# Kernel tuning notes

Measured on AMD Instinct MI355X. Metric: run time of the kernel, lower is better.

Reference implementation:

```python
import jax, jax.numpy as jnp
import numpy as np
import math

B, S, E = 2, 2048, 1024
NH, NKV, HD = 16, 4, 64
GATE_CH = 12

def _rope(x, cos, sin):
    h = x.shape[-1] // 2
    x1, x2 = x[..., :h], x[..., h:]
    return jnp.concatenate((x1 * cos + x2 * sin, x1 * -sin + x2 * cos), axis=-1)

def _rms_norm(x):
    eps = jnp.finfo(x.dtype).eps
    return x * jax.lax.rsqrt(jnp.mean(x * x, axis=-1, keepdims=True) + eps)

def setup_inputs() -> dict:
    key = jax.random.key(0)
    ks = jax.random.split(key, 9)
    x = jax.random.normal(ks[0], (B, S, E), dtype=jnp.float32)
    ve = jax.random.normal(ks[1], (B, S, NKV * HD), dtype=jnp.float32)
    t = jnp.arange(S, dtype=jnp.float32)[:, None]
    inv_freq = 1.0 / (10000.0 ** (jnp.arange(0, HD // 2, dtype=jnp.float32) / (HD // 2)))
    ang = t * inv_freq[None, :]
    cos = jnp.cos(ang)[None, :, None, :]  # (1,S,1,HD//2)
    sin = jnp.sin(ang)[None, :, None, :]
    attn_mask = jnp.tril(jnp.ones((S, S), dtype=bool))[None, None]  # causal (1,1,S,S)
    sc = 0.02
    Wq = jax.random.normal(ks[2], (NH * HD, E), dtype=jnp.float32) * sc
    Wk = jax.random.normal(ks[3], (NKV * HD, E), dtype=jnp.float32) * sc
    Wv = jax.random.normal(ks[4], (NKV * HD, E), dtype=jnp.float32) * sc
    Wproj = jax.random.normal(ks[5], (E, E), dtype=jnp.float32) * sc
    Wgate = jax.random.normal(ks[6], (NKV, GATE_CH), dtype=jnp.float32) * sc
    return {"x": x, "ve": ve, "cos": cos, "sin": sin, "attn_mask": attn_mask,
            "Wq": Wq, "Wk": Wk, "Wv": Wv, "Wproj": Wproj, "Wgate": Wgate}

def reference(x, ve, cos, sin, attn_mask, Wq, Wk, Wv, Wproj, Wgate):
    b, s, _ = x.shape
    q = (x @ Wq.T).reshape(b, s, NH, HD)
    k = (x @ Wk.T).reshape(b, s, NKV, HD)
    v = (x @ Wv.T).reshape(b, s, NKV, HD)
    # value-embedding gating
    gate = 3.0 * jax.nn.sigmoid(x[..., :GATE_CH] @ Wgate.T)  # (b,s,NKV)
    v = v + gate[..., None] * ve.reshape(b, s, NKV, HD)
    # RoPE + QK-RMSNorm
    q = _rms_norm(_rope(q, cos, sin)) * 1.2
    k = _rms_norm(_rope(k, cos, sin)) * 1.2
    # GQA: repeat KV heads
    rep = NH // NKV
    k = jnp.repeat(k, rep, axis=2)
    v = jnp.repeat(v, rep, axis=2)
    q = q.transpose(0, 2, 1, 3)  # (b,h,s,d)
    k = k.transpose(0, 2, 1, 3)
    v = v.transpose(0, 2, 1, 3)
    scores = jnp.einsum('bhqd,bhkd->bhqk', q, k) / math.sqrt(HD)
    scores = jnp.where(attn_mask, scores, jnp.finfo(scores.dtype).min)
    attn = jax.nn.softmax(scores, axis=-1)
    y = jnp.einsum('bhqk,bhkd->bhqd', attn, v)
    y = y.transpose(0, 2, 1, 3).reshape(b, s, NH * HD)
    return y @ Wproj.T
```

## Files before the change

kernel.cpp:

```cpp
#include <hip/hip_runtime.h>
#include <hip/hip_bf16.h>
#include <math.h>

typedef short bf16x8 __attribute__((ext_vector_type(8)));
typedef float f32x4 __attribute__((ext_vector_type(4)));

#define LROW 72
#define NSPLIT 3

__device__ __forceinline__ unsigned short f2bf(float f) {
  union { float f; unsigned int u; } v; v.f = f;
  unsigned int u = v.u;
  unsigned int r = (u + 0x7fffu + ((u >> 16) & 1u)) >> 16;
  return (unsigned short)r;
}
__device__ __forceinline__ float bf2f(unsigned short u) {
  return __uint_as_float((unsigned)u << 16);
}

#if __has_builtin(__builtin_amdgcn_global_load_lds)
#define HAVE_GLD 1
__device__ __forceinline__ void gld16(const void* g, void* l) {
  __builtin_amdgcn_global_load_lds(
      (const __attribute__((address_space(1))) unsigned int*)g,
      (__attribute__((address_space(3))) unsigned int*)l, 16, 0, 0);
}
#else
#define HAVE_GLD 0
#endif

__global__ __launch_bounds__(256) void cvt_all_kernel(const float* __restrict__ x,
                                                      const float* __restrict__ Wq,
                                                      const float* __restrict__ Wk,
                                                      const float* __restrict__ Wv,
                                                      const float* __restrict__ Wproj,
                                                      unsigned short* __restrict__ xb,
                                                      unsigned short* __restrict__ wqkv,
                                                      unsigned short* __restrict__ wpj) {
  int blk = blockIdx.x;
  const float* src;
  unsigned short* dst;
  if (blk < 4096)      { src = x + (size_t)blk * 1024;            dst = xb + (size_t)blk * 1024; }
  else if (blk < 5120) { src = Wq + (size_t)(blk - 4096) * 1024;  dst = wqkv + (size_t)(blk - 4096) * 1024; }
  else if (blk < 5376) { src = Wk + (size_t)(blk - 5120) * 1024;  dst = wqkv + (size_t)(blk - 4096) * 1024; }
  else if (blk < 5632) { src = Wv + (size_t)(blk - 5376) * 1024;  dst = wqkv + (size_t)(blk - 4096) * 1024; }
  else                 { src = Wproj + (size_t)(blk - 5632) * 1024; dst = wpj + (size_t)(blk - 5632) * 1024; }
  int i = threadIdx.x;
  float4 v = ((const float4*)src)[i];
  ushort4 o;
  o.x = f2bf(v.x); o.y = f2bf(v.y); o.z = f2bf(v.z); o.w = f2bf(v.w);
  ((ushort4*)dst)[i] = o;
}

__global__ __launch_bounds__(256) void gemm_qkv_kernel(const unsigned short* __restrict__ A,
                                                       const unsigned short* __restrict__ B,
                                                       const float* __restrict__ ve,
                                                       const float* __restrict__ cosb,
                                                       const float* __restrict__ sinb,
                                                       const float* __restrict__ wgate,
                                                       unsigned short* __restrict__ Q,
                                                       unsigned short* __restrict__ Kd,
                                                       unsigned short* __restrict__ Vt) {
  __shared__ unsigned short As[64 * 64];
  __shared__ unsigned short Bs[128 * 64];
  __shared__ float gLDS[128];
  const int K = 1024;
  int tid = threadIdx.x;
  int wave = tid >> 6, lane = tid & 63, l15 = lane & 15, quad = lane >> 4;
  int wm = (wave >> 1) * 32, wn = (wave & 1) * 64;
  int n0 = blockIdx.x * 128, m0 = blockIdx.y * 64;
  if (n0 >= 1280 && tid < 128) {
    int rl = tid & 63, khl = tid >> 6;
    int kh = ((n0 >> 6) - 20) + khl;
    float dot = 0.f;
#pragma unroll
    for (int jj = 0; jj < 12; jj++)
      dot += bf2f(A[(size_t)(m0 + rl) * 1024 + jj]) * wgate[kh * 12 + jj];
    gLDS[khl * 64 + rl] = 3.0f / (1.0f + __expf(-dot));
  }
  f32x4 acc[2][4];
#pragma unroll
  for (int i = 0; i < 2; i++)
#pragma unroll
    for (int j = 0; j < 4; j++) acc[i][j] = (f32x4){0.f, 0.f, 0.f, 0.f};
  int srow = lane >> 3;
  int scol = ((lane & 7) ^ srow) * 8;
  for (int k0 = 0; k0 < K; k0 += 64) {
    __syncthreads();
#if HAVE_GLD
#pragma unroll
    for (int j = 0; j < 2; j++) {
      int row = wave * 16 + j * 8;
      gld16(A + (size_t)(m0 + row + srow) * K + k0 + scol, As + row * 64 + lane * 8);
    }
#pragma unroll
    for (int j = 0; j < 4; j++) {
      int row = wave * 32 + j * 8;
      gld16(B + (size_t)(n0 + row + srow) * K + k0 + scol, Bs + row * 64 + lane * 8);
    }
#else
#pragma unroll
    for (int j = 0; j < 2; j++) {
      int row = wave * 16 + j * 8;
      *(float4*)(As + row * 64 + lane * 8) = *(const float4*)(A + (size_t)(m0 + row + srow) * K + k0 + scol);
    }
#pragma unroll
    for (int j = 0; j < 4; j++) {
      int row = wave * 32 + j * 8;
      *(float4*)(Bs + row * 64 + lane * 8) = *(const float4*)(B + (size_t)(n0 + row + srow) * K + k0 + scol);
    }
#endif
    __syncthreads();
#pragma unroll
    for (int s = 0; s < 2; s++) {
      bf16x8 af[2], bf[4];
#pragma unroll
      for (int i = 0; i < 2; i++)
        af[i] = *(const bf16x8*)(As + (wm + i * 16 + l15) * 64 + (((s * 4 + quad) ^ (l15 & 7)) * 8));
#pragma unroll
      for (int j = 0; j < 4; j++)
        bf[j] = *(const bf16x8*)(Bs + (wn + j * 16 + l15) * 64 + (((s * 4 + quad) ^ (l15 & 7)) * 8));
#pragma unroll
      for (int i = 0; i < 2; i++)
#pragma unroll
        for (int j = 0; j < 4; j++)
          acc[i][j] = __builtin_amdgcn_mfma_f32_16x16x32_bf16(af[i], bf[j], acc[i][j], 0, 0, 0);
    }
  }
  int hs = (n0 + wn) >> 6;
  if (hs < 20) {
    bool isq = hs < 16;
    float postscale = isq ? 0.216404256f : 1.2f;
#pragma unroll
    for (int i = 0; i < 2; i++) {
#pragma unroll
      for (int r = 0; r < 4; r++) {
        int row = m0 + wm + i * 16 + quad * 4 + r;
        int s = row & 2047, b = row >> 11;
        float c0 = cosb[s * 32 + l15],      s0 = sinb[s * 32 + l15];
        float c1 = cosb[s * 32 + 16 + l15], s1 = sinb[s * 32 + 16 + l15];
        float v0 = acc[i][0][r], v1 = acc[i][1][r], v2 = acc[i][2][r], v3 = acc[i][3][r];
        float n0v = fmaf(v0, c0,  v2 * s0);
        float n1v = fmaf(v1, c1,  v3 * s1);
        float n2v = fmaf(v2, c0, -v0 * s0);
        float n3v = fmaf(v3, c1, -v1 * s1);
        float ss = (n0v * n0v + n1v * n1v) + (n2v * n2v + n3v * n3v);
        ss += __shfl_xor(ss, 1, 64); ss += __shfl_xor(ss, 2, 64);
        ss += __shfl_xor(ss, 4, 64); ss += __shfl_xor(ss, 8, 64);
        float sc = rsqrtf(ss * (1.0f / 64.0f) + 1.1920929e-07f) * postscale;
        unsigned short* dp = isq ? Q + ((size_t)(b * 16 + hs) * 2048 + s) * 64
                                 : Kd + ((size_t)(b * 4 + hs - 16) * 2048 + s) * 64;
        dp[l15]      = f2bf(n0v * sc);
        dp[16 + l15] = f2bf(n1v * sc);
        dp[32 + l15] = f2bf(n2v * sc);
        dp[48 + l15] = f2bf(n3v * sc);
      }
    }
  } else {
    int kh = hs - 20;
#pragma unroll
    for (int i = 0; i < 2; i++) {
#pragma unroll
      for (int r = 0; r < 4; r++) {
        int rl = wm + i * 16 + quad * 4 + r;
        int row = m0 + rl, s = row & 2047, b = row >> 11;
        float g = gLDS[(wave & 1) * 64 + rl];
        const float* vep = ve + (size_t)row * 256 + kh * 64;
        unsigned short* vp = Vt + ((size_t)(b * 4 + kh) * 64) * 2048 + s;
#pragma unroll
        for (int j = 0; j < 4; j++) {
          float vv = fmaf(g, vep[j * 16 + l15], acc[i][j][r]);
          vp[(size_t)(j * 16 + l15) * 2048] = f2bf(vv);
        }
      }
    }
  }
}

__global__ __launch_bounds__(256) void flash_kernel(const unsigned short* __restrict__ Q,
                                                    const unsigned short* __restrict__ K,
                                                    const unsigned short* __restrict__ Vt,
                                                    unsigned short* __restrict__ accP,
                                                    float* __restrict__ lP) {
  __shared__ unsigned short Ks[64 * 64];
  __shared__ unsigned short Vs[64 * 64];
  __shared__ unsigned short Ps[4 * 16 * LROW];
  int pair = blockIdx.x, h = blockIdx.y, bc = blockIdx.z;
  int b = bc / NSPLIT, c = bc % NSPLIT;
  int hb = b * 16 + h;
  int kh = h >> 2;
  int tid = threadIdx.x, wave = tid >> 6, lane = tid & 63, l15 = lane & 15, quad = lane >> 4;
  int l7 = l15 & 7;
  const unsigned short* Kg = K + (size_t)(b * 4 + kh) * 2048 * 64;
  const unsigned short* Vg = Vt + (size_t)(b * 4 + kh) * 64 * 2048;
  unsigned short* Pw = Ps + wave * 16 * LROW;
  int row0 = tid >> 3, col8 = (tid & 7) * 8;
  int dchunk = (((tid & 7) ^ (row0 & 7)) * 8);

#pragma unroll
  for (int half = 0; half < 2; half++) {
    int qt = (half == 0) ? pair : 31 - pair;
    int c0t = ((qt + 1) * c) / NSPLIT;
    int c1t = ((qt + 1) * (c + 1)) / NSPLIT;
    int q0 = qt * 64;
    const unsigned short* Qp = Q + (((size_t)hb * 2048) + q0 + wave * 16 + l15) * 64;
    bf16x8 qf0 = *(const bf16x8*)(Qp + quad * 8);
    bf16x8 qf1 = *(const bf16x8*)(Qp + 32 + quad * 8);
    f32x4 acc[4];
#pragma unroll
    for (int i = 0; i < 4; i++) acc[i] = (f32x4){0.f, 0.f, 0.f, 0.f};
    float l_lane = 0.f;

    if (c1t > c0t) {
      int kf = c0t * 64;
      float4 pk0 = *(const float4*)(Kg + (size_t)(kf + row0) * 64 + col8);
      float4 pk1 = *(const float4*)(Kg + (size_t)(kf + row0 + 32) * 64 + col8);
      float4 pv0 = *(const float4*)(Vg + (size_t)row0 * 2048 + kf + col8);
      float4 pv1 = *(const float4*)(Vg + (size_t)(row0 + 32) * 2048 + kf + col8);

      for (int kt = c0t; kt < c1t; kt++) {
        int k0 = kt * 64;
        __syncthreads();
        *(float4*)(Ks + row0 * 64 + dchunk) = pk0;
        *(float4*)(Ks + (row0 + 32) * 64 + dchunk) = pk1;
        *(float4*)(Vs + row0 * 64 + dchunk) = pv0;
        *(float4*)(Vs + (row0 + 32) * 64 + dchunk) = pv1;
        if (kt + 1 < c1t) {
          int kn = k0 + 64;
          pk0 = *(const float4*)(Kg + (size_t)(kn + row0) * 64 + col8);
          pk1 = *(const float4*)(Kg + (size_t)(kn + row0 + 32) * 64 + col8);
          pv0 = *(const float4*)(Vg + (size_t)row0 * 2048 + kn + col8);
          pv1 = *(const float4*)(Vg + (size_t)(row0 + 32) * 2048 + kn + col8);
        }
        __syncthreads();

        f32x4 sv[4];
#pragma unroll
        for (int mt = 0; mt < 4; mt++) {
          sv[mt] = (f32x4){0.f, 0.f, 0.f, 0.f};
          bf16x8 k0f = *(const bf16x8*)(Ks + (mt * 16 + l15) * 64 + ((quad ^ l7) * 8));
          sv[mt] = __builtin_amdgcn_mfma_f32_16x16x32_bf16(k0f, qf0, sv[mt], 0, 0, 0);
          bf16x8 k1f = *(const bf16x8*)(Ks + (mt * 16 + l15) * 64 + (((4 + quad) ^ l7) * 8));
          sv[mt] = __builtin_amdgcn_mfma_f32_16x16x32_bf16(k1f, qf1, sv[mt], 0, 0, 0);
        }
        if (kt == qt) {
          int qg = q0 + wave * 16 + l15;
#pragma unroll
          for (int mt = 0; mt < 4; mt++) {
            int kg = k0 + mt * 16 + quad * 4;
#pragma unroll
            for (int r = 0; r < 4; r++)
              if (kg + r > qg) sv[mt][r] = -1e30f;
          }
        }
#pragma unroll
        for (int mt = 0; mt < 4; mt++) {
          float p0 = __builtin_amdgcn_exp2f(sv[mt][0]);
          float p1 = __builtin_amdgcn_exp2f(sv[mt][1]);
          float p2 = __builtin_amdgcn_exp2f(sv[mt][2]);
          float p3 = __builtin_amdgcn_exp2f(sv[mt][3]);
          l_lane += (p0 + p1) + (p2 + p3);
          unsigned int lo = __builtin_amdgcn_perm(__float_as_uint(p1), __float_as_uint(p0), 0x07060302u);
          unsigned int hi = __builtin_amdgcn_perm(__float_as_uint(p3), __float_as_uint(p2), 0x07060302u);
          *(uint2*)(Pw + l15 * LROW + mt * 16 + quad * 4) = make_uint2(lo, hi);
        }
#pragma unroll
        for (int step = 0; step < 2; step++) {
          bf16x8 pa = *(const bf16x8*)(Pw + l15 * LROW + step * 32 + quad * 8);
#pragma unroll
          for (int nt = 0; nt < 4; nt++) {
            bf16x8 vb = *(const bf16x8*)(Vs + (nt * 16 + l15) * 64 + (((step * 4 + quad) ^ l7) * 8));
            acc[nt] = __builtin_amdgcn_mfma_f32_16x16x32_bf16(pa, vb, acc[nt], 0, 0, 0);
          }
        }
      }
    }
    l_lane += __shfl_xor(l_lane, 16, 64);
    l_lane += __shfl_xor(l_lane, 32, 64);

    size_t slot = (size_t)(c * 32 + hb) * 2048 + q0 + wave * 16;
    if (lane < 16) lP[slot + l15] = l_lane;
    unsigned short* aP = accP + slot * 64;
#pragma unroll
    for (int r = 0; r < 4; r++)
#pragma unroll
      for (int nt = 0; nt < 4; nt++)
        aP[(size_t)(quad * 4 + r) * 64 + nt * 16 + l15] = f2bf(acc[nt][r]);
  }
}

__global__ __launch_bounds__(256) void merge_kernel(const unsigned short* __restrict__ accP,
                                                    const float* __restrict__ lP,
                                                    unsigned short* __restrict__ Y) {
  int t = blockIdx.x * 256 + threadIdx.x;
  int d4 = (t & 15) * 4;
  int q  = (t >> 4) & 2047;
  int hb = t >> 15;
  const size_t CSTR = (size_t)32 * 2048 * 64;
  size_t pi = ((size_t)hb * 2048 + q) * 64 + d4;
  float y0 = 0.f, y1 = 0.f, y2 = 0.f, y3 = 0.f, l = 0.f;
#pragma unroll
  for (int c = 0; c < NSPLIT; c++) {
    ushort4 a = *(const ushort4*)(accP + pi + c * CSTR);
    y0 += bf2f(a.x); y1 += bf2f(a.y); y2 += bf2f(a.z); y3 += bf2f(a.w);
    l += lP[c * 65536 + hb * 2048 + q];
  }
  float inv = 1.f / l;
  ushort4 o;
  o.x = f2bf(y0 * inv); o.y = f2bf(y1 * inv); o.z = f2bf(y2 * inv); o.w = f2bf(y3 * inv);
  int b = hb >> 4, hh = hb & 15;
  *(ushort4*)(Y + ((size_t)(b * 2048 + q) * 1024) + hh * 64 + d4) = o;
}

__global__ __launch_bounds__(256) void gemm_proj_kernel(const unsigned short* __restrict__ A,
                                                        const unsigned short* __restrict__ B,
                                                        float* __restrict__ C) {
  __shared__ unsigned short As[128 * 64];
  __shared__ unsigned short Bs[64 * 64];
  const int K = 1024, N = 1024;
  int tid = threadIdx.x;
  int wave = tid >> 6, lane = tid & 63, l15 = lane & 15, quad = lane >> 4;
  int wm = (wave >> 1) * 64, wn = (wave & 1) * 32;
  int n0 = blockIdx.x * 64, m0 = blockIdx.y * 128;
  f32x4 acc[4][2];
#pragma unroll
  for (int i = 0; i < 4; i++)
#pragma unroll
    for (int j = 0; j < 2; j++) acc[i][j] = (f32x4){0.f, 0.f, 0.f, 0.f};
  int srow = lane >> 3;
  int scol = ((lane & 7) ^ srow) * 8;
  for (int k0 = 0; k0 < K; k0 += 64) {
    __syncthreads();
#if HAVE_GLD
#pragma unroll
    for (int j = 0; j < 4; j++) {
      int row = wave * 32 + j * 8;
      gld16(A + (size_t)(m0 + row + srow) * K + k0 + scol, As + row * 64 + lane * 8);
    }
#pragma unroll
    for (int j = 0; j < 2; j++) {
      int row = wave * 16 + j * 8;
      gld16(B + (size_t)(n0 + row + srow) * K + k0 + scol, Bs + row * 64 + lane * 8);
    }
#else
#pragma unroll
    for (int j = 0; j < 4; j++) {
      int row = wave * 32 + j * 8;
      *(float4*)(As + row * 64 + lane * 8) = *(const float4*)(A + (size_t)(m0 + row + srow) * K + k0 + scol);
    }
#pragma unroll
    for (int j = 0; j < 2; j++) {
      int row = wave * 16 + j * 8;
      *(float4*)(Bs + row * 64 + lane * 8) = *(const float4*)(B + (size_t)(n0 + row + srow) * K + k0 + scol);
    }
#endif
    __syncthreads();
#pragma unroll
    for (int s = 0; s < 2; s++) {
      bf16x8 af[4], bf[2];
#pragma unroll
      for (int i = 0; i < 4; i++)
        af[i] = *(const bf16x8*)(As + (wm + i * 16 + l15) * 64 + (((s * 4 + quad) ^ (l15 & 7)) * 8));
#pragma unroll
      for (int j = 0; j < 2; j++)
        bf[j] = *(const bf16x8*)(Bs + (wn + j * 16 + l15) * 64 + (((s * 4 + quad) ^ (l15 & 7)) * 8));
#pragma unroll
      for (int i = 0; i < 4; i++)
#pragma unroll
        for (int j = 0; j < 2; j++)
          acc[i][j] = __builtin_amdgcn_mfma_f32_16x16x32_bf16(af[i], bf[j], acc[i][j], 0, 0, 0);
    }
  }
#pragma unroll
  for (int i = 0; i < 4; i++)
#pragma unroll
    for (int j = 0; j < 2; j++)
#pragma unroll
      for (int r = 0; r < 4; r++)
        C[(size_t)(m0 + wm + i * 16 + quad * 4 + r) * N + n0 + wn + j * 16 + l15] = acc[i][j][r];
}

extern "C" void kernel_launch(void* const* d_in, const int* in_sizes, int n_in,
                              void* d_out, int out_size, void* d_ws, size_t ws_size,
                              hipStream_t stream) {
  const float* x     = (const float*)d_in[0];
  const float* ve    = (const float*)d_in[1];
  const float* cosb  = (const float*)d_in[2];
  const float* sinb  = (const float*)d_in[3];
  const float* Wq    = (const float*)d_in[5];
  const float* Wk    = (const float*)d_in[6];
  const float* Wv    = (const float*)d_in[7];
  const float* Wproj = (const float*)d_in[8];
  const float* Wgate = (const float*)d_in[9];
  float* out = (float*)d_out;
  char* ws = (char*)d_ws;

  size_t o = 0;
  unsigned short* xb   = (unsigned short*)(ws + o); o += (size_t)4096 * 1024 * 2;
  unsigned short* wqkv = (unsigned short*)(ws + o); o += (size_t)1536 * 1024 * 2;
  unsigned short* wpj  = (unsigned short*)(ws + o); o += (size_t)1024 * 1024 * 2;
  unsigned short* Qb   = (unsigned short*)(ws + o); o += (size_t)2 * 16 * 2048 * 64 * 2;
  unsigned short* Kb   = (unsigned short*)(ws + o); o += (size_t)2 * 4 * 2048 * 64 * 2;
  unsigned short* Vb   = (unsigned short*)(ws + o); o += (size_t)2 * 4 * 2048 * 64 * 2;
  unsigned short* Yb   = (unsigned short*)(ws + o); o += (size_t)4096 * 1024 * 2;
  unsigned short* accP = (unsigned short*)(ws + o); o += (size_t)NSPLIT * 32 * 2048 * 64 * 2;
  float*          lP   = (float*)(ws + o);          o += (size_t)NSPLIT * 32 * 2048 * 4;

  hipLaunchKernelGGL(cvt_all_kernel, dim3(6656), dim3(256), 0, stream,
                     x, Wq, Wk, Wv, Wproj, xb, wqkv, wpj);
  hipLaunchKernelGGL(gemm_qkv_kernel, dim3(12, 64), dim3(256), 0, stream,
                     xb, wqkv, ve, cosb, sinb, Wgate, Qb, Kb, Vb);
  hipLaunchKernelGGL(flash_kernel, dim3(16, 16, 2 * NSPLIT), dim3(256), 0, stream,
                     Qb, Kb, Vb, accP, lP);
  hipLaunchKernelGGL(merge_kernel, dim3(4096), dim3(256), 0, stream, accP, lP, Yb);
  hipLaunchKernelGGL(gemm_proj_kernel, dim3(16, 32), dim3(256), 0, stream, Yb, wpj, out);
}
```

Before: 177.6 us.

## Enlarge flash attention query tile to 128 rows per block

Each flash block now handles a 128-row query tile, with each wave owning 32 rows as two 16-row fragments that share every K/V tile loaded into LDS. This halves the grid and the number of K/V loads per query row, and skips fully masked key tiles for each wave. It also adds s_setprio around the MFMA sections and a launch_bounds occupancy hint. In exchange, register use rises, there are fewer blocks for load balancing, and the causal split is coarser.

Measured after the change: 176.0 us. No clear change (-0.8%).

```diff
diff --git a/kernel.cpp b/kernel.cpp
--- a/kernel.cpp
+++ b/kernel.cpp
@@ -177,14 +177,14 @@
   }
 }
 
-__global__ __launch_bounds__(256) void flash_kernel(const unsigned short* __restrict__ Q,
-                                                    const unsigned short* __restrict__ K,
-                                                    const unsigned short* __restrict__ Vt,
-                                                    unsigned short* __restrict__ accP,
-                                                    float* __restrict__ lP) {
+__global__ __launch_bounds__(256, 3) void flash_kernel(const unsigned short* __restrict__ Q,
+                                                       const unsigned short* __restrict__ K,
+                                                       const unsigned short* __restrict__ Vt,
+                                                       unsigned short* __restrict__ accP,
+                                                       float* __restrict__ lP) {
   __shared__ unsigned short Ks[64 * 64];
   __shared__ unsigned short Vs[64 * 64];
-  __shared__ unsigned short Ps[4 * 16 * LROW];
+  __shared__ unsigned short Ps[4 * 32 * LROW];
   int pair = blockIdx.x, h = blockIdx.y, bc = blockIdx.z;
   int b = bc / NSPLIT, c = bc % NSPLIT;
   int hb = b * 16 + h;
@@ -193,23 +193,31 @@
   int l7 = l15 & 7;
   const unsigned short* Kg = K + (size_t)(b * 4 + kh) * 2048 * 64;
   const unsigned short* Vg = Vt + (size_t)(b * 4 + kh) * 64 * 2048;
-  unsigned short* Pw = Ps + wave * 16 * LROW;
+  unsigned short* Pw = Ps + wave * 32 * LROW;
   int row0 = tid >> 3, col8 = (tid & 7) * 8;
   int dchunk = (((tid & 7) ^ (row0 & 7)) * 8);
 
 #pragma unroll
   for (int half = 0; half < 2; half++) {
-    int qt = (half == 0) ? pair : 31 - pair;
-    int c0t = ((qt + 1) * c) / NSPLIT;
-    int c1t = ((qt + 1) * (c + 1)) / NSPLIT;
-    int q0 = qt * 64;
-    const unsigned short* Qp = Q + (((size_t)hb * 2048) + q0 + wave * 16 + l15) * 64;
-    bf16x8 qf0 = *(const bf16x8*)(Qp + quad * 8);
-    bf16x8 qf1 = *(const bf16x8*)(Qp + 32 + quad * 8);
-    f32x4 acc[4];
-#pragma unroll
-    for (int i = 0; i < 4; i++) acc[i] = (f32x4){0.f, 0.f, 0.f, 0.f};
-    float l_lane = 0.f;
+    int qt = (half == 0) ? pair : 15 - pair;
+    int NT = 2 * qt + 2;
+    int c0t = (NT * c) / NSPLIT;
+    int c1t = (NT * (c + 1)) / NSPLIT;
+    int q0 = qt * 128;
+    int qw = q0 + wave * 32;
+    const unsigned short* Qp = Q + (((size_t)hb * 2048) + qw + l15) * 64;
+    bf16x8 qf[2][2];
+    qf[0][0] = *(const bf16x8*)(Qp + quad * 8);
+    qf[0][1] = *(const bf16x8*)(Qp + 32 + quad * 8);
+    qf[1][0] = *(const bf16x8*)(Qp + 16 * 64 + quad * 8);
+    qf[1][1] = *(const bf16x8*)(Qp + 16 * 64 + 32 + quad * 8);
+    f32x4 acc[4][2];
+#pragma unroll
+    for (int i = 0; i < 4; i++) {
+      acc[i][0] = (f32x4){0.f, 0.f, 0.f, 0.f};
+      acc[i][1] = (f32x4){0.f, 0.f, 0.f, 0.f};
+    }
+    float ll[2] = {0.f, 0.f};
 
     if (c1t > c0t) {
       int kf = c0t * 64;
@@ -234,58 +242,85 @@
         }
         __syncthreads();
 
-        f32x4 sv[4];
-#pragma unroll
-        for (int mt = 0; mt < 4; mt++) {
-          sv[mt] = (f32x4){0.f, 0.f, 0.f, 0.f};
-          bf16x8 k0f = *(const bf16x8*)(Ks + (mt * 16 + l15) * 64 + ((quad ^ l7) * 8));
-          sv[mt] = __builtin_amdgcn_mfma_f32_16x16x32_bf16(k0f, qf0, sv[mt], 0, 0, 0);
-          bf16x8 k1f = *(const bf16x8*)(Ks + (mt * 16 + l15) * 64 + (((4 + quad) ^ l7) * 8));
-          sv[mt] = __builtin_amdgcn_mfma_f32_16x16x32_bf16(k1f, qf1, sv[mt], 0, 0, 0);
-        }
-        if (kt == qt) {
-          int qg = q0 + wave * 16 + l15;
+        if (k0 <= qw + 31) {
+          f32x4 sv[4][2];
 #pragma unroll
           for (int mt = 0; mt < 4; mt++) {
-            int kg = k0 + mt * 16 + quad * 4;
-#pragma unroll
-            for (int r = 0; r < 4; r++)
-              if (kg + r > qg) sv[mt][r] = -1e30f;
+            sv[mt][0] = (f32x4){0.f, 0.f, 0.f, 0.f};
+            sv[mt][1] = (f32x4){0.f, 0.f, 0.f, 0.f};
           }
-        }
-#pragma unroll
-        for (int mt = 0; mt < 4; mt++) {
-          float p0 = __builtin_amdgcn_exp2f(sv[mt][0]);
-          float p1 = __builtin_amdgcn_exp2f(sv[mt][1]);
-          float p2 = __builtin_amdgcn_exp2f(sv[mt][2]);
-          float p3 = __builtin_amdgcn_exp2f(sv[mt][3]);
-          l_lane += (p0 + p1) + (p2 + p3);
-          unsigned int lo = __builtin_amdgcn_perm(__float_as_uint(p1), __float_as_uint(p0), 0x07060302u);
-          unsigned int hi = __builtin_amdgcn_perm(__float_as_uint(p3), __float_as_uint(p2), 0x07060302u);
-          *(uint2*)(Pw + l15 * LROW + mt * 16 + quad * 4) = make_uint2(lo, hi);
-        }
-#pragma unroll
-        for (int step = 0; step < 2; step++) {
-          bf16x8 pa = *(const bf16x8*)(Pw + l15 * LROW + step * 32 + quad * 8);
-#pragma unroll
-          for (int nt = 0; nt < 4; nt++) {
-            bf16x8 vb = *(const bf16x8*)(Vs + (nt * 16 + l15) * 64 + (((step * 4 + quad) ^ l7) * 8));
-            acc[nt] = __builtin_amdgcn_mfma_f32_16x16x32_bf16(pa, vb, acc[nt], 0, 0, 0);
+          __builtin_amdgcn_s_setprio(1);
+#pragma unroll
+          for (int mt = 0; mt < 4; mt++) {
+            bf16x8 k0f = *(const bf16x8*)(Ks + (mt * 16 + l15) * 64 + ((quad ^ l7) * 8));
+            bf16x8 k1f = *(const bf16x8*)(Ks + (mt * 16 + l15) * 64 + (((4 + quad) ^ l7) * 8));
+            sv[mt][0] = __builtin_amdgcn_mfma_f32_16x16x32_bf16(k0f, qf[0][0], sv[mt][0], 0, 0, 0);
+            sv[mt][0] = __builtin_amdgcn_mfma_f32_16x16x32_bf16(k1f, qf[0][1], sv[mt][0], 0, 0, 0);
+            sv[mt][1] = __builtin_amdgcn_mfma_f32_16x16x32_bf16(k0f, qf[1][0], sv[mt][1], 0, 0, 0);
+            sv[mt][1] = __builtin_amdgcn_mfma_f32_16x16x32_bf16(k1f, qf[1][1], sv[mt][1], 0, 0, 0);
           }
+          __builtin_amdgcn_s_setprio(0);
+          if (k0 + 63 > qw) {
+#pragma unroll
+            for (int f = 0; f < 2; f++) {
+              int qg = qw + f * 16 + l15;
+#pragma unroll
+              for (int mt = 0; mt < 4; mt++) {
+                int kg = k0 + mt * 16 + quad * 4;
+#pragma unroll
+                for (int r = 0; r < 4; r++)
+                  if (kg + r > qg) sv[mt][f][r] = -1e30f;
+              }
+            }
+          }
+#pragma unroll
+          for (int f = 0; f < 2; f++) {
+#pragma unroll
+            for (int mt = 0; mt < 4; mt++) {
+              float p0 = __builtin_amdgcn_exp2f(sv[mt][f][0]);
+              float p1 = __builtin_amdgcn_exp2f(sv[mt][f][1]);
+              float p2 = __builtin_amdgcn_exp2f(sv[mt][f][2]);
+              float p3 = __builtin_amdgcn_exp2f(sv[mt][f][3]);
+              ll[f] += (p0 + p1) + (p2 + p3);
+              unsigned int lo = __builtin_amdgcn_perm(__float_as_uint(p1), __float_as_uint(p0), 0x07060302u);
+              unsigned int hi = __builtin_amdgcn_perm(__float_as_uint(p3), __float_as_uint(p2), 0x07060302u);
+              *(uint2*)(Pw + (f * 16 + l15) * LROW + mt * 16 + quad * 4) = make_uint2(lo, hi);
+            }
+          }
+          __builtin_amdgcn_s_setprio(1);
+#pragma unroll
+          for (int step = 0; step < 2; step++) {
+            bf16x8 pa0 = *(const bf16x8*)(Pw + l15 * LROW + step * 32 + quad * 8);
+            bf16x8 pa1 = *(const bf16x8*)(Pw + (16 + l15) * LROW + step * 32 + quad * 8);
+#pragma unroll
+            for (int nt = 0; nt < 4; nt++) {
+              bf16x8 vb = *(const bf16x8*)(Vs + (nt * 16 + l15) * 64 + (((step * 4 + quad) ^ l7) * 8));
+              acc[nt][0] = __builtin_amdgcn_mfma_f32_16x16x32_bf16(pa0, vb, acc[nt][0], 0, 0, 0);
+              acc[nt][1] = __builtin_amdgcn_mfma_f32_16x16x32_bf16(pa1, vb, acc[nt][1], 0, 0, 0);
+            }
+          }
+          __builtin_amdgcn_s_setprio(0);
         }
       }
     }
-    l_lane += __shfl_xor(l_lane, 16, 64);
-    l_lane += __shfl_xor(l_lane, 32, 64);
-
-    size_t slot = (size_t)(c * 32 + hb) * 2048 + q0 + wave * 16;
-    if (lane < 16) lP[slot + l15] = l_lane;
+    ll[0] += __shfl_xor(ll[0], 16, 64);
+    ll[0] += __shfl_xor(ll[0], 32, 64);
+    ll[1] += __shfl_xor(ll[1], 16, 64);
+    ll[1] += __shfl_xor(ll[1], 32, 64);
+
+    size_t slot = (size_t)(c * 32 + hb) * 2048 + qw;
+    if (lane < 16) {
+      lP[slot + l15] = ll[0];
+      lP[slot + 16 + l15] = ll[1];
+    }
     unsigned short* aP = accP + slot * 64;
 #pragma unroll
-    for (int r = 0; r < 4; r++)
-#pragma unroll
-      for (int nt = 0; nt < 4; nt++)
-        aP[(size_t)(quad * 4 + r) * 64 + nt * 16 + l15] = f2bf(acc[nt][r]);
+    for (int f = 0; f < 2; f++)
+#pragma unroll
+      for (int r = 0; r < 4; r++)
+#pragma unroll
+        for (int nt = 0; nt < 4; nt++)
+          aP[(size_t)(f * 16 + quad * 4 + r) * 64 + nt * 16 + l15] = f2bf(acc[nt][f][r]);
   }
 }
 
@@ -410,7 +445,7 @@
                      x, Wq, Wk, Wv, Wproj, xb, wqkv, wpj);
   hipLaunchKernelGGL(gemm_qkv_kernel, dim3(12, 64), dim3(256), 0, stream,
                      xb, wqkv, ve, cosb, sinb, Wgate, Qb, Kb, Vb);
-  hipLaunchKernelGGL(flash_kernel, dim3(16, 16, 2 * NSPLIT), dim3(256), 0, stream,
+  hipLaunchKernelGGL(flash_kernel, dim3(8, 16, 2 * NSPLIT), dim3(256), 0, stream,
                      Qb, Kb, Vb, accP, lP);
   hipLaunchKernelGGL(merge_kernel, dim3(4096), dim3(256), 0, stream, accP, lP, Yb);
   hipLaunchKernelGGL(gemm_proj_kernel, dim3(16, 32), dim3(256), 0, stream, Yb, wpj, out);
```

## Drop split-KV and merge kernel; normalize in flash epilogue, add setprio around MFMAs

Applied to the files above, without the earlier changes.

Removes the 3-way KV split and the separate merge kernel, so each flash block handles the full causal key range for its paired query tiles and writes normalized bf16 output straight into Y. This removes the partial-accumulator writes and reads, the merge launch and one bf16 rounding of the partial sums. It also wraps the MFMA sections in s_setprio to favor matrix-issue waves. In exchange the grid shrinks from 1536 to 512 blocks, which lowers parallelism and occupancy on a many-CU device.

After: 173.6 us. 1.02x faster.

```diff
diff --git a/kernel.cpp b/kernel.cpp
--- a/kernel.cpp
+++ b/kernel.cpp
@@ -6,7 +6,6 @@
 typedef float f32x4 __attribute__((ext_vector_type(4)));
 
 #define LROW 72
-#define NSPLIT 3
 
 __device__ __forceinline__ unsigned short f2bf(float f) {
   union { float f; unsigned int u; } v; v.f = f;
@@ -180,13 +179,11 @@
 __global__ __launch_bounds__(256) void flash_kernel(const unsigned short* __restrict__ Q,
                                                     const unsigned short* __restrict__ K,
                                                     const unsigned short* __restrict__ Vt,
-                                                    unsigned short* __restrict__ accP,
-                                                    float* __restrict__ lP) {
+                                                    unsigned short* __restrict__ Y) {
   __shared__ unsigned short Ks[64 * 64];
   __shared__ unsigned short Vs[64 * 64];
   __shared__ unsigned short Ps[4 * 16 * LROW];
-  int pair = blockIdx.x, h = blockIdx.y, bc = blockIdx.z;
-  int b = bc / NSPLIT, c = bc % NSPLIT;
+  int pair = blockIdx.x, h = blockIdx.y, b = blockIdx.z;
   int hb = b * 16 + h;
   int kh = h >> 2;
   int tid = threadIdx.x, wave = tid >> 6, lane = tid & 63, l15 = lane & 15, quad = lane >> 4;
@@ -200,8 +197,7 @@
 #pragma unroll
   for (int half = 0; half < 2; half++) {
     int qt = (half == 0) ? pair : 31 - pair;
-    int c0t = ((qt + 1) * c) / NSPLIT;
-    int c1t = ((qt + 1) * (c + 1)) / NSPLIT;
+    int NT = qt + 1;
     int q0 = qt * 64;
     const unsigned short* Qp = Q + (((size_t)hb * 2048) + q0 + wave * 16 + l15) * 64;
     bf16x8 qf0 = *(const bf16x8*)(Qp + quad * 8);
@@ -211,21 +207,20 @@
     for (int i = 0; i < 4; i++) acc[i] = (f32x4){0.f, 0.f, 0.f, 0.f};
     float l_lane = 0.f;
 
-    if (c1t > c0t) {
-      int kf = c0t * 64;
-      float4 pk0 = *(const float4*)(Kg + (size_t)(kf + row0) * 64 + col8);
-      float4 pk1 = *(const float4*)(Kg + (size_t)(kf + row0 + 32) * 64 + col8);
-      float4 pv0 = *(const float4*)(Vg + (size_t)row0 * 2048 + kf + col8);
-      float4 pv1 = *(const float4*)(Vg + (size_t)(row0 + 32) * 2048 + kf + col8);
-
-      for (int kt = c0t; kt < c1t; kt++) {
+    {
+      float4 pk0 = *(const float4*)(Kg + (size_t)row0 * 64 + col8);
+      float4 pk1 = *(const float4*)(Kg + (size_t)(row0 + 32) * 64 + col8);
+      float4 pv0 = *(const float4*)(Vg + (size_t)row0 * 2048 + col8);
+      float4 pv1 = *(const float4*)(Vg + (size_t)(row0 + 32) * 2048 + col8);
+
+      for (int kt = 0; kt < NT; kt++) {
         int k0 = kt * 64;
         __syncthreads();
         *(float4*)(Ks + row0 * 64 + dchunk) = pk0;
         *(float4*)(Ks + (row0 + 32) * 64 + dchunk) = pk1;
         *(float4*)(Vs + row0 * 64 + dchunk) = pv0;
         *(float4*)(Vs + (row0 + 32) * 64 + dchunk) = pv1;
-        if (kt + 1 < c1t) {
+        if (kt + 1 < NT) {
           int kn = k0 + 64;
           pk0 = *(const float4*)(Kg + (size_t)(kn + row0) * 64 + col8);
           pk1 = *(const float4*)(Kg + (size_t)(kn + row0 + 32) * 64 + col8);
@@ -235,6 +230,7 @@
         __syncthreads();
 
         f32x4 sv[4];
+        __builtin_amdgcn_s_setprio(1);
 #pragma unroll
         for (int mt = 0; mt < 4; mt++) {
           sv[mt] = (f32x4){0.f, 0.f, 0.f, 0.f};
@@ -243,6 +239,7 @@
           bf16x8 k1f = *(const bf16x8*)(Ks + (mt * 16 + l15) * 64 + (((4 + quad) ^ l7) * 8));
           sv[mt] = __builtin_amdgcn_mfma_f32_16x16x32_bf16(k1f, qf1, sv[mt], 0, 0, 0);
         }
+        __builtin_amdgcn_s_setprio(0);
         if (kt == qt) {
           int qg = q0 + wave * 16 + l15;
 #pragma unroll
@@ -264,6 +261,7 @@
           unsigned int hi = __builtin_amdgcn_perm(__float_as_uint(p3), __float_as_uint(p2), 0x07060302u);
           *(uint2*)(Pw + l15 * LROW + mt * 16 + quad * 4) = make_uint2(lo, hi);
         }
+        __builtin_amdgcn_s_setprio(1);
 #pragma unroll
         for (int step = 0; step < 2; step++) {
           bf16x8 pa = *(const bf16x8*)(Pw + l15 * LROW + step * 32 + quad * 8);
@@ -273,43 +271,22 @@
             acc[nt] = __builtin_amdgcn_mfma_f32_16x16x32_bf16(pa, vb, acc[nt], 0, 0, 0);
           }
         }
+        __builtin_amdgcn_s_setprio(0);
       }
     }
     l_lane += __shfl_xor(l_lane, 16, 64);
     l_lane += __shfl_xor(l_lane, 32, 64);
 
-    size_t slot = (size_t)(c * 32 + hb) * 2048 + q0 + wave * 16;
-    if (lane < 16) lP[slot + l15] = l_lane;
-    unsigned short* aP = accP + slot * 64;
-#pragma unroll
-    for (int r = 0; r < 4; r++)
+#pragma unroll
+    for (int r = 0; r < 4; r++) {
+      float inv = 1.0f / __shfl(l_lane, quad * 4 + r, 16);
+      int qrow = q0 + wave * 16 + quad * 4 + r;
+      unsigned short* yp = Y + ((size_t)(b * 2048 + qrow) * 1024) + h * 64;
 #pragma unroll
       for (int nt = 0; nt < 4; nt++)
-        aP[(size_t)(quad * 4 + r) * 64 + nt * 16 + l15] = f2bf(acc[nt][r]);
-  }
-}
-
-__global__ __launch_bounds__(256) void merge_kernel(const unsigned short* __restrict__ accP,
-                                                    const float* __restrict__ lP,
-                                                    unsigned short* __restrict__ Y) {
-  int t = blockIdx.x * 256 + threadIdx.x;
-  int d4 = (t & 15) * 4;
-  int q  = (t >> 4) & 2047;
-  int hb = t >> 15;
-  const size_t CSTR = (size_t)32 * 2048 * 64;
-  size_t pi = ((size_t)hb * 2048 + q) * 64 + d4;
-  float y0 = 0.f, y1 = 0.f, y2 = 0.f, y3 = 0.f, l = 0.f;
-#pragma unroll
-  for (int c = 0; c < NSPLIT; c++) {
-    ushort4 a = *(const ushort4*)(accP + pi + c * CSTR);
-    y0 += bf2f(a.x); y1 += bf2f(a.y); y2 += bf2f(a.z); y3 += bf2f(a.w);
-    l += lP[c * 65536 + hb * 2048 + q];
-  }
-  float inv = 1.f / l;
-  ushort4 o;
-  o.x = f2bf(y0 * inv); o.y = f2bf(y1 * inv); o.z = f2bf(y2 * inv); o.w = f2bf(y3 * inv);
-  int b = hb >> 4, hh = hb & 15;
-  *(ushort4*)(Y + ((size_t)(b * 2048 + q) * 1024) + hh * 64 + d4) = o;
+        yp[nt * 16 + l15] = f2bf(acc[nt][r] * inv);
+    }
+  }
 }
 
 __global__ __launch_bounds__(256) void gemm_proj_kernel(const unsigned short* __restrict__ A,
@@ -403,15 +380,12 @@
   unsigned short* Kb   = (unsigned short*)(ws + o); o += (size_t)2 * 4 * 2048 * 64 * 2;
   unsigned short* Vb   = (unsigned short*)(ws + o); o += (size_t)2 * 4 * 2048 * 64 * 2;
   unsigned short* Yb   = (unsigned short*)(ws + o); o += (size_t)4096 * 1024 * 2;
-  unsigned short* accP = (unsigned short*)(ws + o); o += (size_t)NSPLIT * 32 * 2048 * 64 * 2;
-  float*          lP   = (float*)(ws + o);          o += (size_t)NSPLIT * 32 * 2048 * 4;
 
   hipLaunchKernelGGL(cvt_all_kernel, dim3(6656), dim3(256), 0, stream,
                      x, Wq, Wk, Wv, Wproj, xb, wqkv, wpj);
   hipLaunchKernelGGL(gemm_qkv_kernel, dim3(12, 64), dim3(256), 0, stream,
                      xb, wqkv, ve, cosb, sinb, Wgate, Qb, Kb, Vb);
-  hipLaunchKernelGGL(flash_kernel, dim3(16, 16, 2 * NSPLIT), dim3(256), 0, stream,
-                     Qb, Kb, Vb, accP, lP);
-  hipLaunchKernelGGL(merge_kernel, dim3(4096), dim3(256), 0, stream, accP, lP, Yb);
+  hipLaunchKernelGGL(flash_kernel, dim3(16, 16, 2), dim3(256), 0, stream,
+                     Qb, Kb, Vb, Yb);
   hipLaunchKernelGGL(gemm_proj_kernel, dim3(16, 32), dim3(256), 0, stream, Yb, wpj, out);
 }
```
